# Performance work log

Measured on AMD Instinct MI355X. Metric: run time of the kernel, lower is better.

Reference implementation:

```python
import jax, jax.numpy as jnp
import numpy as np

B, N = 16, 286
EMB_DIM = 4
CLOUD_DIM = 4
NB = 3          # number_of_basis
HID = 150       # radial MLP hidden width
RADIUS = 3.0    # neighbor radius / max_radius of cosine basis
FF = 512


def sp5(x):
    # torch Softplus(beta=5)
    return jax.nn.softplus(5.0 * x) / 5.0


def cosine_basis(r):
    # e3nn CosineBasisModel embedding: cos^2 bumps on [0, RADIUS]
    centers = jnp.linspace(0.0, RADIUS, NB)
    step = centers[1] - centers[0]
    d = (r[..., None] - centers) / step                     # [B,N,N,NB]
    return jnp.cos(jnp.pi / 2 * d) ** 2 * (jnp.abs(d) < 1.0)


def cloud_conv(feats, dist, mask, ws, bs, dim_out):
    # radial MLP on pairwise distances -> per-pair [dim_out, dim_in] kernel (l=0 only)
    x = cosine_basis(dist)
    for w, b in zip(ws[:-1], bs[:-1]):
        x = sp5(x @ w + b)
    R = x @ ws[-1] + bs[-1]                                 # [B,N,N,dim_out*dim_in]
    b_, n_ = dist.shape[0], dist.shape[1]
    k = R.reshape(b_, n_, n_, dim_out, -1) * mask[..., None, None]
    nb = jnp.maximum(mask.sum(-1), 1.0)                     # neighbors per atom [B,N]
    out = jnp.einsum('zabij,zbj->zai', k, feats) / jnp.sqrt(nb)[..., None]
    return out


def setup_inputs() -> dict:
    key = jax.random.key(0)
    ks = jax.random.split(key, 32)
    xyz = jax.random.normal(ks[0], (B, N, 3), dtype=jnp.float32)
    Z = jax.random.randint(ks[1], (B, N), 0, 11)
    emb = jax.random.normal(ks[2], (11, EMB_DIM), dtype=jnp.float32)
    inp = {'xyz': xyz, 'Z': Z, 'emb': emb}
    # radial MLPs per cloud: 3 -> 150 -> 150 -> 150 -> dim_out*dim_in (=16)
    dims = [NB, HID, HID, HID, CLOUD_DIM * CLOUD_DIM]
    ki = 3
    for c in range(2):
        for l in range(4):
            w = jax.random.normal(ks[ki], (dims[l], dims[l + 1]), dtype=jnp.float32) / np.sqrt(dims[l])
            b = jnp.zeros((dims[l + 1],), dtype=jnp.float32)
            inp[f'c{c}_w{l}'] = w
            inp[f'c{c}_b{l}'] = b
            ki += 1
    cloud_out = CLOUD_DIM * 2  # cloud_dim * cloud_order^2 * nclouds = 8
    inp['fc_w'] = jax.random.normal(ks[ki], (cloud_out, FF), dtype=jnp.float32) / np.sqrt(cloud_out); ki += 1
    inp['fc_b'] = jnp.zeros((FF,), dtype=jnp.float32)
    inp['bn_g'] = jnp.ones((FF,), dtype=jnp.float32)
    inp['bn_b'] = jnp.zeros((FF,), dtype=jnp.float32)
    inp['out_w'] = jax.random.normal(ks[ki], (FF, 1), dtype=jnp.float32) / np.sqrt(FF); ki += 1
    inp['out_b'] = jnp.zeros((1,), dtype=jnp.float32)
    return inp


def reference(xyz, Z, emb,
              c0_w0, c0_b0, c0_w1, c0_b1, c0_w2, c0_b2, c0_w3, c0_b3,
              c1_w0, c1_b0, c1_w1, c1_b1, c1_w2, c1_b2, c1_w3, c1_b3,
              fc_w, fc_b, bn_g, bn_b, out_w, out_b):
    feats = emb[Z]                                          # [B,N,emb_dim]
    diff = xyz[:, :, None, :] - xyz[:, None, :, :]
    dist = jnp.sqrt(jnp.sum(diff * diff, -1) + 1e-12)       # [B,N,N]
    mask = (dist < RADIUS).astype(feats.dtype)
    f1 = cloud_conv(feats, dist, mask,
                    [c0_w0, c0_w1, c0_w2, c0_w3], [c0_b0, c0_b1, c0_b2, c0_b3], CLOUD_DIM)
    f2 = cloud_conv(f1, dist, mask,
                    [c1_w0, c1_w1, c1_w2, c1_w3], [c1_b0, c1_b1, c1_b2, c1_b3], CLOUD_DIM)
    feats_cat = jnp.concatenate([f1, f2], axis=2)           # [B,N,8]
    # lp_pool2d(norm=2, kernel=(N,1)) == L2 norm over atom dim
    pooled = jnp.sqrt(jnp.sum(feats_cat ** 2, axis=1))      # [B,8]
    h = jax.nn.softplus(pooled @ fc_w + fc_b)
    mean = h.mean(0)
    var = h.var(0)
    h = jax.nn.softplus((h - mean) / jnp.sqrt(var + 1e-5) * bn_g + bn_b)
    return jax.nn.sigmoid(h @ out_w + out_b)[:, 0]          # [B]
```

## Files before the change

### kernel.cpp

```cpp
#include <hip/hip_runtime.h>
#include <hip/hip_bf16.h>
#include <math.h>

#define B_SZ   16
#define N_ATOM 286
#define NT     1024
#define HIDW   150
#define FF_DIM 512
#define EPB    8

__device__ __forceinline__ float softplus_f(float x) {
  return fmaxf(x, 0.0f) + log1pf(expf(-fabsf(x)));
}
__device__ __forceinline__ float sp5_f(float x) {
  float t = 5.0f * x;
  return (fmaxf(t, 0.0f) + log1pf(expf(-fabsf(t)))) * 0.2f;
}

__device__ __forceinline__ void hidden_layer(
    const float* __restrict__ W, const float* __restrict__ bias,
    const float* __restrict__ src, float* __restrict__ dst,
    int lane, int e0) {
  const int o2 = 128 + lane;
  const int o2c = (o2 < HIDW) ? o2 : (HIDW - 1);
  float acc00 = bias[lane],     acc01 = acc00;
  float acc10 = bias[64 + lane], acc11 = acc10;
  float acc20 = bias[o2c],      acc21 = acc20;
  #pragma unroll 5
  for (int i = 0; i < HIDW; ++i) {
    const float2 hv = *(const float2*)(src + i * EPB + e0);
    const float* __restrict__ Wr = W + i * HIDW;
    float wv0 = Wr[lane];
    float wv1 = Wr[64 + lane];
    int idx2 = i * HIDW + o2;
    idx2 = (idx2 <= HIDW * HIDW - 1) ? idx2 : (HIDW * HIDW - 1);
    float wv2 = W[idx2];
    acc00 = __builtin_fmaf(hv.x, wv0, acc00); acc01 = __builtin_fmaf(hv.y, wv0, acc01);
    acc10 = __builtin_fmaf(hv.x, wv1, acc10); acc11 = __builtin_fmaf(hv.y, wv1, acc11);
    acc20 = __builtin_fmaf(hv.x, wv2, acc20); acc21 = __builtin_fmaf(hv.y, wv2, acc21);
  }
  *(float2*)(dst + lane * EPB + e0)        = make_float2(sp5_f(acc00), sp5_f(acc01));
  *(float2*)(dst + (64 + lane) * EPB + e0) = make_float2(sp5_f(acc10), sp5_f(acc11));
  if (o2 < HIDW)
    *(float2*)(dst + o2 * EPB + e0)        = make_float2(sp5_f(acc20), sp5_f(acc21));
}

__global__ __launch_bounds__(256) void table_kernel(
    const float* __restrict__ a_w0, const float* __restrict__ a_b0,
    const float* __restrict__ a_w1, const float* __restrict__ a_b1,
    const float* __restrict__ a_w2, const float* __restrict__ a_b2,
    const float* __restrict__ a_w3, const float* __restrict__ a_b3,
    const float* __restrict__ c_w0, const float* __restrict__ c_b0,
    const float* __restrict__ c_w1, const float* __restrict__ c_b1,
    const float* __restrict__ c_w2, const float* __restrict__ c_b2,
    const float* __restrict__ c_w3, const float* __restrict__ c_b3,
    float* __restrict__ tab0, float* __restrict__ tab1) {
  __shared__ float actA[HIDW * EPB];
  __shared__ float actB[HIDW * EPB];

  const int nblk = NT / EPB;
  const int cloud = (blockIdx.x >= nblk) ? 1 : 0;
  const int blk   = blockIdx.x - cloud * nblk;
  const float* w0 = cloud ? c_w0 : a_w0;  const float* b0 = cloud ? c_b0 : a_b0;
  const float* w1 = cloud ? c_w1 : a_w1;  const float* b1 = cloud ? c_b1 : a_b1;
  const float* w2 = cloud ? c_w2 : a_w2;  const float* b2 = cloud ? c_b2 : a_b2;
  const float* w3 = cloud ? c_w3 : a_w3;  const float* b3 = cloud ? c_b3 : a_b3;
  float* table = cloud ? tab1 : tab0;

  const int tid  = threadIdx.x;
  const int lane = tid & 63;
  const int wave = __builtin_amdgcn_readfirstlane(tid >> 6);
  const int e0   = wave * 2;
  const int gbase = blk * EPB;

  float x0[3], x1[3];
  #pragma unroll
  for (int k = 0; k < 3; ++k) {
    float r0 = 3.0f * (float)(gbase + e0)     / (float)(NT - 1);
    float r1 = 3.0f * (float)(gbase + e0 + 1) / (float)(NT - 1);
    float d0 = (r0 - 1.5f * (float)k) * (1.0f / 1.5f);
    float d1 = (r1 - 1.5f * (float)k) * (1.0f / 1.5f);
    float c0 = cosf(1.57079632679489662f * d0);
    float c1 = cosf(1.57079632679489662f * d1);
    x0[k] = (fabsf(d0) < 1.0f) ? c0 * c0 : 0.0f;
    x1[k] = (fabsf(d1) < 1.0f) ? c1 * c1 : 0.0f;
  }

  #pragma unroll
  for (int c = 0; c < 3; ++c) {
    int o = lane + 64 * c;
    int oc = (o < HIDW) ? o : (HIDW - 1);
    float w00 = w0[oc], w01 = w0[HIDW + oc], w02 = w0[2 * HIDW + oc], bb = b0[oc];
    float h0 = sp5_f(bb + x0[0] * w00 + x0[1] * w01 + x0[2] * w02);
    float h1 = sp5_f(bb + x1[0] * w00 + x1[1] * w01 + x1[2] * w02);
    if (o < HIDW) *(float2*)(actA + o * EPB + e0) = make_float2(h0, h1);
  }

  hidden_layer(w1, b1, actA, actB, lane, e0);
  hidden_layer(w2, b2, actB, actA, lane, e0);

  {
    const int o  = lane & 15;
    const int ig = lane >> 4;
    float a0 = 0.f, a1 = 0.f;
    for (int i = ig; i < HIDW; i += 4) {
      float wv = w3[i * 16 + o];
      float h0 = actA[i * EPB + e0];
      float h1 = actA[i * EPB + e0 + 1];
      a0 = __builtin_fmaf(h0, wv, a0);
      a1 = __builtin_fmaf(h1, wv, a1);
    }
    a0 += __shfl_xor(a0, 16, 64); a0 += __shfl_xor(a0, 32, 64);
    a1 += __shfl_xor(a1, 16, 64); a1 += __shfl_xor(a1, 32, 64);
    if (lane < 16) {
      float bb = b3[o];
      table[(size_t)(gbase + e0)     * 16 + o] = a0 + bb;
      table[(size_t)(gbase + e0 + 1) * 16 + o] = a1 + bb;
    }
  }
}

__global__ __launch_bounds__(256) void conv_kernel(
    const float* __restrict__ xyz, const int* __restrict__ Z,
    const float* __restrict__ emb, const float* __restrict__ feats_in,
    const float* __restrict__ table, float* __restrict__ f_out, int gather) {
  const int wave = threadIdx.x >> 6;
  const int lane = threadIdx.x & 63;
  const int row = blockIdx.x * 4 + wave;
  if (row >= B_SZ * N_ATOM) return;
  const int z = row / N_ATOM, a = row % N_ATOM;
  const float* xz = xyz + (size_t)z * N_ATOM * 3;
  const float ax = xz[a * 3 + 0], ay = xz[a * 3 + 1], az = xz[a * 3 + 2];

  float acc[4] = {0.f, 0.f, 0.f, 0.f};
  float cnt = 0.f;
  for (int b = lane; b < N_ATOM; b += 64) {
    float bx = xz[b * 3 + 0], by = xz[b * 3 + 1], bz = xz[b * 3 + 2];
    float dx = ax - bx, dy = ay - by, dz = az - bz;
    float r = sqrtf(dx * dx + dy * dy + dz * dz + 1e-12f);
    if (r < 3.0f) {
      cnt += 1.0f;
      float t = r * ((float)(NT - 1) / 3.0f);
      int idx = (int)t;
      if (idx > NT - 2) idx = NT - 2;
      float fr = t - (float)idx;
      const float4* T = (const float4*)(table + (size_t)idx * 16);
      float4 fb;
      if (gather) {
        int zi = Z[z * N_ATOM + b];
        fb = *(const float4*)(emb + (size_t)zi * 4);
      } else {
        fb = *(const float4*)(feats_in + ((size_t)z * N_ATOM + b) * 4);
      }
      #pragma unroll
      for (int i = 0; i < 4; ++i) {
        float4 r0 = T[i], r1 = T[i + 4];
        float v0 = r0.x + fr * (r1.x - r0.x);
        float v1 = r0.y + fr * (r1.y - r0.y);
        float v2 = r0.z + fr * (r1.z - r0.z);
        float v3 = r0.w + fr * (r1.w - r0.w);
        acc[i] += v0 * fb.x + v1 * fb.y + v2 * fb.z + v3 * fb.w;
      }
    }
  }
  #pragma unroll
  for (int m = 32; m > 0; m >>= 1) {
    #pragma unroll
    for (int i = 0; i < 4; ++i) acc[i] += __shfl_xor(acc[i], m, 64);
    cnt += __shfl_xor(cnt, m, 64);
  }
  if (lane == 0) {
    float nb = cnt < 1.0f ? 1.0f : cnt;
    float sc = 1.0f / sqrtf(nb);
    float4 o;
    o.x = acc[0] * sc; o.y = acc[1] * sc; o.z = acc[2] * sc; o.w = acc[3] * sc;
    *(float4*)(f_out + (size_t)row * 4) = o;
  }
}

__global__ __launch_bounds__(512) void tail_kernel(
    const float* __restrict__ f1, const float* __restrict__ f2,
    const float* __restrict__ fc_w, const float* __restrict__ fc_b,
    const float* __restrict__ bn_g, const float* __restrict__ bn_b,
    const float* __restrict__ out_w, const float* __restrict__ out_b,
    float* __restrict__ out) {
  __shared__ float pooled[16][8];
  __shared__ float part[8][16];
  const int tid = threadIdx.x;

  {
    int pair = tid >> 2;
    int sub  = tid & 3;
    int z = pair >> 3, c = pair & 7;
    const float* src = (c < 4) ? f1 : f2;
    int cc = c & 3;
    float s = 0.f;
    for (int a = sub; a < N_ATOM; a += 4) {
      float v = src[((size_t)z * N_ATOM + a) * 4 + cc];
      s += v * v;
    }
    s += __shfl_xor(s, 1, 64);
    s += __shfl_xor(s, 2, 64);
    if (sub == 0) pooled[z][c] = sqrtf(s);
  }
  __syncthreads();

  const int f = tid;
  float hv[16];
  float mean = 0.f;
  #pragma unroll
  for (int z = 0; z < 16; ++z) {
    float a = fc_b[f];
    #pragma unroll
    for (int c = 0; c < 8; ++c) a += pooled[z][c] * fc_w[c * FF_DIM + f];
    hv[z] = softplus_f(a);
    mean += hv[z];
  }
  mean *= (1.0f / 16.0f);
  float var = 0.f;
  #pragma unroll
  for (int z = 0; z < 16; ++z) { float d = hv[z] - mean; var += d * d; }
  var *= (1.0f / 16.0f);
  float istd = 1.0f / sqrtf(var + 1e-5f);
  float g = bn_g[f], bb = bn_b[f], ow = out_w[f];
  float contrib[16];
  #pragma unroll
  for (int z = 0; z < 16; ++z)
    contrib[z] = softplus_f((hv[z] - mean) * istd * g + bb) * ow;

  const int lane = tid & 63, wv = tid >> 6;
  #pragma unroll
  for (int m = 32; m > 0; m >>= 1) {
    #pragma unroll
    for (int z = 0; z < 16; ++z) contrib[z] += __shfl_xor(contrib[z], m, 64);
  }
  if (lane == 0) {
    #pragma unroll
    for (int z = 0; z < 16; ++z) part[wv][z] = contrib[z];
  }
  __syncthreads();
  if (tid < 16) {
    float s = out_b[0];
    #pragma unroll
    for (int w8 = 0; w8 < 8; ++w8) s += part[w8][tid];
    out[tid] = 1.0f / (1.0f + expf(-s));
  }
}

extern "C" void kernel_launch(void* const* d_in, const int* in_sizes, int n_in,
                              void* d_out, int out_size, void* d_ws, size_t ws_size,
                              hipStream_t stream) {
  const float* xyz = (const float*)d_in[0];
  const int*   Z   = (const int*)d_in[1];
  const float* emb = (const float*)d_in[2];
  const float* c0[8]; const float* c1[8];
  for (int i = 0; i < 8; ++i) {
    c0[i] = (const float*)d_in[3 + i];
    c1[i] = (const float*)d_in[11 + i];
  }
  const float* fc_w  = (const float*)d_in[19];
  const float* fc_b  = (const float*)d_in[20];
  const float* bn_g  = (const float*)d_in[21];
  const float* bn_b  = (const float*)d_in[22];
  const float* out_w = (const float*)d_in[23];
  const float* out_b = (const float*)d_in[24];
  float* out = (float*)d_out;

  float* wsf = (float*)d_ws;
  const size_t TAB_ELEMS = (size_t)NT * 16;
  float* t0 = wsf;
  float* t1 = t0 + TAB_ELEMS;
  float* f1 = t1 + TAB_ELEMS;
  float* f2 = f1 + (size_t)B_SZ * N_ATOM * 4;

  table_kernel<<<2 * (NT / EPB), 256, 0, stream>>>(
      c0[0], c0[1], c0[2], c0[3], c0[4], c0[5], c0[6], c0[7],
      c1[0], c1[1], c1[2], c1[3], c1[4], c1[5], c1[6], c1[7], t0, t1);

  const int conv_blocks = (B_SZ * N_ATOM + 3) / 4;
  conv_kernel<<<conv_blocks, 256, 0, stream>>>(xyz, Z, emb, (const float*)nullptr,
                                               t0, f1, 1);
  conv_kernel<<<conv_blocks, 256, 0, stream>>>(xyz, Z, emb, f1,
                                               t1, f2, 0);

  tail_kernel<<<1, 512, 0, stream>>>(f1, f2, fc_w, fc_b, bn_g, bn_b,
                                     out_w, out_b, out);
}
```

Before: 203.8 us.

## Repack hidden MLP weights with padded bias rows and store tables in fp16

Adds a prep kernel that copies the two hidden-layer weight matrices per cloud into a padded 152-wide layout with the bias folded in as an extra row. Each lane then computes four outputs with float4 weight loads instead of three strided scalar loads, which means fewer load instructions but only 38 of 64 lanes doing useful work. The radial lookup tables are now stored in half precision, halving the bytes the conv kernels gather. The costs are an extra kernel launch and some fp16 rounding error in the interpolated kernel values.

```diff
diff --git a/kernel.cpp b/kernel.cpp
--- a/kernel.cpp
+++ b/kernel.cpp
@@ -1,5 +1,6 @@
 #include <hip/hip_runtime.h>
 #include <hip/hip_bf16.h>
+#include <hip/hip_fp16.h>
 #include <math.h>
 
 #define B_SZ   16
@@ -7,7 +8,8 @@
 #define NT     1024
 #define HIDW   150
 #define FF_DIM 512
-#define EPB    8
+#define WPAD   152
+#define WROWS  151
 
 __device__ __forceinline__ float softplus_f(float x) {
   return fmaxf(x, 0.0f) + log1pf(expf(-fabsf(x)));
@@ -17,61 +19,71 @@
   return (fmaxf(t, 0.0f) + log1pf(expf(-fabsf(t)))) * 0.2f;
 }
 
-__device__ __forceinline__ void hidden_layer(
-    const float* __restrict__ W, const float* __restrict__ bias,
-    const float* __restrict__ src, float* __restrict__ dst,
-    int lane, int e0) {
-  const int o2 = 128 + lane;
-  const int o2c = (o2 < HIDW) ? o2 : (HIDW - 1);
-  float acc00 = bias[lane],     acc01 = acc00;
-  float acc10 = bias[64 + lane], acc11 = acc10;
-  float acc20 = bias[o2c],      acc21 = acc20;
-  #pragma unroll 5
+__global__ __launch_bounds__(256) void prep_kernel(
+    const float* __restrict__ w1a, const float* __restrict__ b1a,
+    const float* __restrict__ w2a, const float* __restrict__ b2a,
+    const float* __restrict__ w1c, const float* __restrict__ b1c,
+    const float* __restrict__ w2c, const float* __restrict__ b2c,
+    float* __restrict__ Wp) {
+  const int m = blockIdx.y;
+  const float* W  = (m == 0) ? w1a : (m == 1) ? w2a : (m == 2) ? w1c : w2c;
+  const float* Bb = (m == 0) ? b1a : (m == 1) ? b2a : (m == 2) ? b1c : b2c;
+  int idx = blockIdx.x * 256 + threadIdx.x;
+  if (idx < WROWS * WPAD) {
+    int i = idx / WPAD, o = idx % WPAD;
+    float v = 0.0f;
+    if (o < HIDW) v = (i < HIDW) ? W[i * HIDW + o] : Bb[o];
+    Wp[(size_t)m * WROWS * WPAD + idx] = v;
+  }
+}
+
+__device__ __forceinline__ void hidden_layer_v2(
+    const float* __restrict__ Wp,
+    const float* __restrict__ src,
+    float* __restrict__ dst,
+    int jj, int e0) {
+  const float4 bb = *(const float4*)(Wp + HIDW * WPAD + 4 * jj);
+  float4 a0 = bb, a1 = bb;
+  #pragma unroll 8
   for (int i = 0; i < HIDW; ++i) {
-    const float2 hv = *(const float2*)(src + i * EPB + e0);
-    const float* __restrict__ Wr = W + i * HIDW;
-    float wv0 = Wr[lane];
-    float wv1 = Wr[64 + lane];
-    int idx2 = i * HIDW + o2;
-    idx2 = (idx2 <= HIDW * HIDW - 1) ? idx2 : (HIDW * HIDW - 1);
-    float wv2 = W[idx2];
-    acc00 = __builtin_fmaf(hv.x, wv0, acc00); acc01 = __builtin_fmaf(hv.y, wv0, acc01);
-    acc10 = __builtin_fmaf(hv.x, wv1, acc10); acc11 = __builtin_fmaf(hv.y, wv1, acc11);
-    acc20 = __builtin_fmaf(hv.x, wv2, acc20); acc21 = __builtin_fmaf(hv.y, wv2, acc21);
-  }
-  *(float2*)(dst + lane * EPB + e0)        = make_float2(sp5_f(acc00), sp5_f(acc01));
-  *(float2*)(dst + (64 + lane) * EPB + e0) = make_float2(sp5_f(acc10), sp5_f(acc11));
-  if (o2 < HIDW)
-    *(float2*)(dst + o2 * EPB + e0)        = make_float2(sp5_f(acc20), sp5_f(acc21));
+    float4 wv = *(const float4*)(Wp + i * WPAD + 4 * jj);
+    float2 h  = *(const float2*)(src + i * 8 + e0);
+    a0.x = __builtin_fmaf(h.x, wv.x, a0.x); a1.x = __builtin_fmaf(h.y, wv.x, a1.x);
+    a0.y = __builtin_fmaf(h.x, wv.y, a0.y); a1.y = __builtin_fmaf(h.y, wv.y, a1.y);
+    a0.z = __builtin_fmaf(h.x, wv.z, a0.z); a1.z = __builtin_fmaf(h.y, wv.z, a1.z);
+    a0.w = __builtin_fmaf(h.x, wv.w, a0.w); a1.w = __builtin_fmaf(h.y, wv.w, a1.w);
+  }
+  *(float2*)(dst + (4 * jj + 0) * 8 + e0) = make_float2(sp5_f(a0.x), sp5_f(a1.x));
+  *(float2*)(dst + (4 * jj + 1) * 8 + e0) = make_float2(sp5_f(a0.y), sp5_f(a1.y));
+  *(float2*)(dst + (4 * jj + 2) * 8 + e0) = make_float2(sp5_f(a0.z), sp5_f(a1.z));
+  *(float2*)(dst + (4 * jj + 3) * 8 + e0) = make_float2(sp5_f(a0.w), sp5_f(a1.w));
 }
 
 __global__ __launch_bounds__(256) void table_kernel(
     const float* __restrict__ a_w0, const float* __restrict__ a_b0,
-    const float* __restrict__ a_w1, const float* __restrict__ a_b1,
-    const float* __restrict__ a_w2, const float* __restrict__ a_b2,
     const float* __restrict__ a_w3, const float* __restrict__ a_b3,
     const float* __restrict__ c_w0, const float* __restrict__ c_b0,
-    const float* __restrict__ c_w1, const float* __restrict__ c_b1,
-    const float* __restrict__ c_w2, const float* __restrict__ c_b2,
     const float* __restrict__ c_w3, const float* __restrict__ c_b3,
-    float* __restrict__ tab0, float* __restrict__ tab1) {
-  __shared__ float actA[HIDW * EPB];
-  __shared__ float actB[HIDW * EPB];
-
-  const int nblk = NT / EPB;
+    const float* __restrict__ Wp,
+    __half* __restrict__ tabh0, __half* __restrict__ tabh1) {
+  __shared__ float actA[WPAD * 8];
+  __shared__ float actB[WPAD * 8];
+
+  const int nblk = NT / 8;
   const int cloud = (blockIdx.x >= nblk) ? 1 : 0;
   const int blk   = blockIdx.x - cloud * nblk;
   const float* w0 = cloud ? c_w0 : a_w0;  const float* b0 = cloud ? c_b0 : a_b0;
-  const float* w1 = cloud ? c_w1 : a_w1;  const float* b1 = cloud ? c_b1 : a_b1;
-  const float* w2 = cloud ? c_w2 : a_w2;  const float* b2 = cloud ? c_b2 : a_b2;
   const float* w3 = cloud ? c_w3 : a_w3;  const float* b3 = cloud ? c_b3 : a_b3;
-  float* table = cloud ? tab1 : tab0;
+  const float* Wp1 = Wp + (size_t)(cloud * 2)     * WROWS * WPAD;
+  const float* Wp2 = Wp + (size_t)(cloud * 2 + 1) * WROWS * WPAD;
+  __half* table = cloud ? tabh1 : tabh0;
 
   const int tid  = threadIdx.x;
   const int lane = tid & 63;
   const int wave = __builtin_amdgcn_readfirstlane(tid >> 6);
   const int e0   = wave * 2;
-  const int gbase = blk * EPB;
+  const int gbase = blk * 8;
+  const int jj = (lane < 38) ? lane : 37;
 
   float x0[3], x1[3];
   #pragma unroll
@@ -93,11 +105,11 @@
     float w00 = w0[oc], w01 = w0[HIDW + oc], w02 = w0[2 * HIDW + oc], bb = b0[oc];
     float h0 = sp5_f(bb + x0[0] * w00 + x0[1] * w01 + x0[2] * w02);
     float h1 = sp5_f(bb + x1[0] * w00 + x1[1] * w01 + x1[2] * w02);
-    if (o < HIDW) *(float2*)(actA + o * EPB + e0) = make_float2(h0, h1);
-  }
-
-  hidden_layer(w1, b1, actA, actB, lane, e0);
-  hidden_layer(w2, b2, actB, actA, lane, e0);
+    if (o < HIDW) *(float2*)(actA + o * 8 + e0) = make_float2(h0, h1);
+  }
+
+  hidden_layer_v2(Wp1, actA, actB, jj, e0);
+  hidden_layer_v2(Wp2, actB, actA, jj, e0);
 
   {
     const int o  = lane & 15;
@@ -105,8 +117,8 @@
     float a0 = 0.f, a1 = 0.f;
     for (int i = ig; i < HIDW; i += 4) {
       float wv = w3[i * 16 + o];
-      float h0 = actA[i * EPB + e0];
-      float h1 = actA[i * EPB + e0 + 1];
+      float h0 = actA[i * 8 + e0];
+      float h1 = actA[i * 8 + e0 + 1];
       a0 = __builtin_fmaf(h0, wv, a0);
       a1 = __builtin_fmaf(h1, wv, a1);
     }
@@ -114,16 +126,25 @@
     a1 += __shfl_xor(a1, 16, 64); a1 += __shfl_xor(a1, 32, 64);
     if (lane < 16) {
       float bb = b3[o];
-      table[(size_t)(gbase + e0)     * 16 + o] = a0 + bb;
-      table[(size_t)(gbase + e0 + 1) * 16 + o] = a1 + bb;
+      table[(size_t)(gbase + e0)     * 16 + o] = __float2half(a0 + bb);
+      table[(size_t)(gbase + e0 + 1) * 16 + o] = __float2half(a1 + bb);
     }
+  }
+}
+
+__device__ __forceinline__ void cvt8(uint4 q, float* out) {
+  const __half2* h = (const __half2*)&q;
+  #pragma unroll
+  for (int k = 0; k < 4; ++k) {
+    float2 f = __half22float2(h[k]);
+    out[2 * k] = f.x; out[2 * k + 1] = f.y;
   }
 }
 
 __global__ __launch_bounds__(256) void conv_kernel(
     const float* __restrict__ xyz, const int* __restrict__ Z,
     const float* __restrict__ emb, const float* __restrict__ feats_in,
-    const float* __restrict__ table, float* __restrict__ f_out, int gather) {
+    const __half* __restrict__ tabh, float* __restrict__ f_out, int gather) {
   const int wave = threadIdx.x >> 6;
   const int lane = threadIdx.x & 63;
   const int row = blockIdx.x * 4 + wave;
@@ -144,7 +165,8 @@
       int idx = (int)t;
       if (idx > NT - 2) idx = NT - 2;
       float fr = t - (float)idx;
-      const float4* T = (const float4*)(table + (size_t)idx * 16);
+      const uint4* Tp = (const uint4*)(tabh + (size_t)idx * 16);
+      uint4 q0 = Tp[0], q1 = Tp[1], q2 = Tp[2], q3 = Tp[3];
       float4 fb;
       if (gather) {
         int zi = Z[z * N_ATOM + b];
@@ -152,13 +174,15 @@
       } else {
         fb = *(const float4*)(feats_in + ((size_t)z * N_ATOM + b) * 4);
       }
+      float r0[16], r1[16];
+      cvt8(q0, r0); cvt8(q1, r0 + 8);
+      cvt8(q2, r1); cvt8(q3, r1 + 8);
       #pragma unroll
       for (int i = 0; i < 4; ++i) {
-        float4 r0 = T[i], r1 = T[i + 4];
-        float v0 = r0.x + fr * (r1.x - r0.x);
-        float v1 = r0.y + fr * (r1.y - r0.y);
-        float v2 = r0.z + fr * (r1.z - r0.z);
-        float v3 = r0.w + fr * (r1.w - r0.w);
+        float v0 = r0[4 * i + 0] + fr * (r1[4 * i + 0] - r0[4 * i + 0]);
+        float v1 = r0[4 * i + 1] + fr * (r1[4 * i + 1] - r0[4 * i + 1]);
+        float v2 = r0[4 * i + 2] + fr * (r1[4 * i + 2] - r0[4 * i + 2]);
+        float v3 = r0[4 * i + 3] + fr * (r1[4 * i + 3] - r0[4 * i + 3]);
         acc[i] += v0 * fb.x + v1 * fb.y + v2 * fb.z + v3 * fb.w;
       }
     }
@@ -267,21 +291,28 @@
   float* out = (float*)d_out;
 
   float* wsf = (float*)d_ws;
-  const size_t TAB_ELEMS = (size_t)NT * 16;
-  float* t0 = wsf;
-  float* t1 = t0 + TAB_ELEMS;
-  float* f1 = t1 + TAB_ELEMS;
+  float* Wp = wsf;
+  float* f1 = Wp + (size_t)4 * WROWS * WPAD;
   float* f2 = f1 + (size_t)B_SZ * N_ATOM * 4;
-
-  table_kernel<<<2 * (NT / EPB), 256, 0, stream>>>(
-      c0[0], c0[1], c0[2], c0[3], c0[4], c0[5], c0[6], c0[7],
-      c1[0], c1[1], c1[2], c1[3], c1[4], c1[5], c1[6], c1[7], t0, t1);
+  __half* tabh0 = (__half*)(f2 + (size_t)B_SZ * N_ATOM * 4);
+  __half* tabh1 = tabh0 + (size_t)NT * 16;
+
+  {
+    dim3 g((WROWS * WPAD + 255) / 256, 4);
+    prep_kernel<<<g, 256, 0, stream>>>(c0[2], c0[3], c0[4], c0[5],
+                                       c1[2], c1[3], c1[4], c1[5], Wp);
+  }
+
+  table_kernel<<<2 * (NT / 8), 256, 0, stream>>>(
+      c0[0], c0[1], c0[6], c0[7],
+      c1[0], c1[1], c1[6], c1[7],
+      Wp, tabh0, tabh1);
 
   const int conv_blocks = (B_SZ * N_ATOM + 3) / 4;
   conv_kernel<<<conv_blocks, 256, 0, stream>>>(xyz, Z, emb, (const float*)nullptr,
-                                               t0, f1, 1);
+                                               tabh0, f1, 1);
   conv_kernel<<<conv_blocks, 256, 0, stream>>>(xyz, Z, emb, f1,
-                                               t1, f2, 0);
+                                               tabh1, f2, 0);
 
   tail_kernel<<<1, 512, 0, stream>>>(f1, f2, fc_w, fc_b, bn_g, bn_b,
                                      out_w, out_b, out);
```

New measurement: 196.7 us. 1.04x faster.
